# Kernel optimization log

Hardware: AMD Instinct MI355X
Metric: run time of the kernel (lower is better)

The kernel has to match this reference:

```python
import jax, jax.numpy as jnp
import numpy as np

N_SRC = 50000
N_DST = 50000
N_EDGES = 1600000
D_IN = 128
K = 8          # num_heads
D_OUT = 16     # out_dim per head (K*D_OUT = 128)
NEG_SLOPE = 0.2


def setup_inputs() -> dict:
    key = jax.random.key(0)
    ks = jax.random.split(key, 8)
    feat_src = jax.random.normal(ks[0], (N_SRC, D_IN), dtype=jnp.float32)
    feat_dst = jax.random.normal(ks[1], (N_DST, D_IN), dtype=jnp.float32)
    W_src = jax.random.normal(ks[2], (D_IN, K * D_OUT), dtype=jnp.float32) * (1.0 / np.sqrt(D_IN))
    b_src = jnp.zeros((K * D_OUT,), dtype=jnp.float32)
    W_dst = jax.random.normal(ks[3], (D_IN, K * D_OUT), dtype=jnp.float32) * (1.0 / np.sqrt(D_IN))
    b_dst = jnp.zeros((K * D_OUT,), dtype=jnp.float32)
    attn_src = jax.random.normal(ks[4], (K, 2 * D_OUT), dtype=jnp.float32) * 0.1
    src_idx = jax.random.randint(ks[5], (N_EDGES,), 0, N_SRC, dtype=jnp.int64)
    dst_idx = jax.random.randint(ks[6], (N_EDGES,), 0, N_DST, dtype=jnp.int64)
    return {"feat_src": feat_src, "feat_dst": feat_dst, "W_src": W_src, "b_src": b_src,
            "W_dst": W_dst, "b_dst": b_dst, "attn_src": attn_src,
            "src_idx": src_idx, "dst_idx": dst_idx}


def reference(feat_src, feat_dst, W_src, b_src, W_dst, b_dst, attn_src, src_idx, dst_idx):
    n_dst = feat_dst.shape[0]
    # feat_drop is identity (p=0). Linear projections, reshape to heads.
    hs = (feat_src @ W_src + b_src).reshape(-1, K, D_OUT)  # [N_src, K, D_out]
    hd = (feat_dst @ W_dst + b_dst).reshape(-1, K, D_OUT)  # [N_dst, K, D_out]
    # per-node attention logits
    el = jnp.sum(hs * attn_src[:, :D_OUT], axis=-1)  # [N_src, K]
    er = jnp.sum(hd * attn_src[:, D_OUT:], axis=-1)  # [N_dst, K]
    # per-edge score: u_add_v then LeakyReLU
    e = el[src_idx] + er[dst_idx]                    # [E, K]
    e = jnp.where(e >= 0, e, NEG_SLOPE * e)
    # edge softmax over incoming edges of each dst node (numerically stable)
    emax = jax.ops.segment_max(e, dst_idx, num_segments=n_dst)
    emax = jnp.where(jnp.isfinite(emax), emax, 0.0)  # handle dsts with no edges
    ee = jnp.exp(e - emax[dst_idx])                  # [E, K]
    esum = jax.ops.segment_sum(ee, dst_idx, num_segments=n_dst)
    a = ee / esum[dst_idx]                           # [E, K]
    # weighted message aggregation: u_mul_e then sum over incoming edges
    m = hs[src_idx] * a[:, :, None]                  # [E, K, D_out]
    out = jax.ops.segment_sum(m, dst_idx, num_segments=n_dst)  # [N_dst, K, D_out]
    return out.reshape(n_dst, K * D_OUT)
```

## Files before the change

### kernel.cpp

```cpp
#include <hip/hip_runtime.h>
#include <hip/hip_bf16.h>

#define NEG_SLOPE 0.2f
#define EPB   8192
#define CAP   4096
#define MAXC  1024

typedef __attribute__((ext_vector_type(8))) short bf16x8;
typedef __attribute__((ext_vector_type(4))) float f32x4;

__device__ __forceinline__ float b2f_lo(unsigned u) { return __uint_as_float(u << 16); }
__device__ __forceinline__ float b2f_hi(unsigned u) { return __uint_as_float(u & 0xffff0000u); }

__device__ __forceinline__ short f2b(float x) {
    unsigned u = __float_as_uint(x);
    unsigned r = (u + 0x7fffu + ((u >> 16) & 1u)) >> 16;
    return (short)r;
}

__global__ __launch_bounds__(256) void pack_kernel(
    const float* __restrict__ W_src, const float* __restrict__ W_dst,
    const float* __restrict__ b_src, const float* __restrict__ b_dst,
    const float* __restrict__ attn,
    uint4* __restrict__ wp_src, uint4* __restrict__ wp_dst,
    float* __restrict__ c_all,
    int* __restrict__ cursor, int nCoarse)
{
    const int e = blockIdx.x * 256 + threadIdx.x;
    if (e < 4608) {
        const int which = e / 2304;
        const int e2 = e % 2304;
        const float* W = which ? W_dst : W_src;
        uint4* wp = which ? wp_dst : wp_src;
        const int aoff = which ? 16 : 0;
        short out[8];
        if (e2 < 2048) {
            const int t = e2 >> 8, q = (e2 >> 6) & 3, l = e2 & 63;
            const int kbase = (l >> 4) * 8 + q * 32;
            const int n = t * 16 + (l & 15);
            #pragma unroll
            for (int j = 0; j < 8; ++j) out[j] = f2b(W[(size_t)(kbase + j) * 128 + n]);
            *(uint4*)&wp[(t * 4 + q) * 64 + l] = *(uint4*)out;
        } else {
            const int e3 = e2 - 2048;
            const int q = e3 >> 6, l = e3 & 63;
            const int kbase = (l >> 4) * 8 + q * 32;
            const int n = l & 15;
            #pragma unroll
            for (int j = 0; j < 8; ++j) {
                float v = 0.f;
                if (n < 8) {
                    for (int dd = 0; dd < 16; ++dd)
                        v += W[(size_t)(kbase + j) * 128 + n * 16 + dd] * attn[n * 32 + aoff + dd];
                }
                out[j] = f2b(v);
            }
            *(uint4*)&wp[(32 + q) * 64 + l] = *(uint4*)out;
        }
    } else if (e < 4624) {
        const int k = e - 4608;
        const int which = k >> 3, kk = k & 7;
        const float* bb = which ? b_dst : b_src;
        const int aoff = which ? 16 : 0;
        float v = 0.f;
        for (int dd = 0; dd < 16; ++dd) v += bb[kk * 16 + dd] * attn[kk * 32 + aoff + dd];
        c_all[k] = v;
    } else if (e < 4624 + nCoarse) {
        const int c = e - 4624;
        cursor[c] = c * CAP;
    }
}

__device__ __forceinline__ void scatter_body(
    const int* __restrict__ src_idx, const int* __restrict__ dst_idx,
    int* __restrict__ cursor, int* __restrict__ coarse,
    int nEdges, int nCoarse, int bx)
{
    __shared__ int lcnt[MAXC];
    __shared__ int lbase[MAXC];
    const int t = threadIdx.x;
    for (int i = t; i < nCoarse; i += 256) lcnt[i] = 0;
    __syncthreads();
    const int e0 = bx * EPB;
    const int e1 = min(e0 + EPB, nEdges);
    for (int e = e0 + t; e < e1; e += 256) atomicAdd(&lcnt[dst_idx[e] >> 6], 1);
    __syncthreads();
    for (int i = t; i < nCoarse; i += 256) {
        const int c = lcnt[i];
        lbase[i] = c ? atomicAdd(&cursor[i], c) : 0;
        lcnt[i] = 0;
    }
    __syncthreads();
    for (int e = e0 + t; e < e1; e += 256) {
        const int d = dst_idx[e];
        const int s = src_idx[e];
        const int bin = d >> 6;
        const int lr = atomicAdd(&lcnt[bin], 1);
        const int pos = lbase[bin] + lr;
        if (pos < (bin + 1) * CAP)
            coarse[pos] = (s << 6) | (d & 63);
    }
}

template<bool STORE_H>
__device__ __forceinline__ void proj_body(
    const float* __restrict__ feat, const uint4* __restrict__ wp,
    const float* __restrict__ b, const float* __restrict__ cvec,
    short* __restrict__ hs_out, float* __restrict__ el_out,
    int N, int bx)
{
    const int t = threadIdx.x;
    const int lane = t & 63;
    const int w = t >> 6;
    const int m  = lane & 15;
    const int q8 = lane >> 4;
    const int row0 = bx * 128 + w * 32;

    f32x4 acc0[9], acc1[9];
    #pragma unroll
    for (int tt = 0; tt < 8; ++tt) {
        const float bn = b[tt * 16 + m];
        acc0[tt] = (f32x4){bn, bn, bn, bn};
        acc1[tt] = (f32x4){bn, bn, bn, bn};
    }
    acc0[8] = (f32x4){0.f, 0.f, 0.f, 0.f};
    acc1[8] = (f32x4){0.f, 0.f, 0.f, 0.f};

    int rowA0 = row0 + m;      if (rowA0 >= N) rowA0 = N - 1;
    int rowA1 = row0 + 16 + m; if (rowA1 >= N) rowA1 = N - 1;
    const float* f0 = feat + (size_t)rowA0 * 128 + q8 * 8;
    const float* f1 = feat + (size_t)rowA1 * 128 + q8 * 8;
    const bf16x8* wpv = (const bf16x8*)wp;

    #pragma unroll
    for (int kc = 0; kc < 4; ++kc) {
        const float4 fa0 = *(const float4*)(f0 + kc * 32);
        const float4 fb0 = *(const float4*)(f0 + kc * 32 + 4);
        const float4 fa1 = *(const float4*)(f1 + kc * 32);
        const float4 fb1 = *(const float4*)(f1 + kc * 32 + 4);
        bf16x8 a0, a1;
        a0[0]=f2b(fa0.x); a0[1]=f2b(fa0.y); a0[2]=f2b(fa0.z); a0[3]=f2b(fa0.w);
        a0[4]=f2b(fb0.x); a0[5]=f2b(fb0.y); a0[6]=f2b(fb0.z); a0[7]=f2b(fb0.w);
        a1[0]=f2b(fa1.x); a1[1]=f2b(fa1.y); a1[2]=f2b(fa1.z); a1[3]=f2b(fa1.w);
        a1[4]=f2b(fb1.x); a1[5]=f2b(fb1.y); a1[6]=f2b(fb1.z); a1[7]=f2b(fb1.w);
        #pragma unroll
        for (int tt = 0; tt < 8; ++tt) {
            const bf16x8 bf = wpv[(tt * 4 + kc) * 64 + lane];
            acc0[tt] = __builtin_amdgcn_mfma_f32_16x16x32_bf16(a0, bf, acc0[tt], 0, 0, 0);
            acc1[tt] = __builtin_amdgcn_mfma_f32_16x16x32_bf16(a1, bf, acc1[tt], 0, 0, 0);
        }
        {
            const bf16x8 bv = wpv[(32 + kc) * 64 + lane];
            acc0[8] = __builtin_amdgcn_mfma_f32_16x16x32_bf16(a0, bv, acc0[8], 0, 0, 0);
            acc1[8] = __builtin_amdgcn_mfma_f32_16x16x32_bf16(a1, bv, acc1[8], 0, 0, 0);
        }
    }

    #pragma unroll
    for (int half = 0; half < 2; ++half) {
        const f32x4* acc = half ? acc1 : acc0;
        const int rbase = row0 + half * 16 + q8 * 4;
        #pragma unroll
        for (int reg = 0; reg < 4; ++reg) {
            const int row = rbase + reg;
            if (row < N) {
                if (STORE_H) {
                    #pragma unroll
                    for (int tt = 0; tt < 8; ++tt)
                        hs_out[(size_t)row * 128 + tt * 16 + m] = f2b(acc[tt][reg]);
                }
                if (m < 8) el_out[(size_t)row * 8 + m] = acc[8][reg] + cvec[m];
            }
        }
    }
}

__global__ __launch_bounds__(256, 2) void fused_kernel(
    const float* __restrict__ feat_src, const float* __restrict__ feat_dst,
    const uint4* __restrict__ wp_src, const uint4* __restrict__ wp_dst,
    const float* __restrict__ b_src, const float* __restrict__ b_dst,
    const float* __restrict__ c_all,
    short* __restrict__ hs, float* __restrict__ el, float* __restrict__ er,
    const int* __restrict__ src_idx, const int* __restrict__ dst_idx,
    int* __restrict__ cursor, int* __restrict__ coarse,
    int n_src, int n_dst, int nEdges, int nCoarse, int nSB, int pSrcBlocks)
{
    int bx = blockIdx.x;
    if (bx < nSB) { scatter_body(src_idx, dst_idx, cursor, coarse, nEdges, nCoarse, bx); return; }
    bx -= nSB;
    if (bx < pSrcBlocks) {
        proj_body<true>(feat_src, wp_src, b_src, c_all, hs, el, n_src, bx);
        return;
    }
    bx -= pSrcBlocks;
    proj_body<false>(feat_dst, wp_dst, b_dst, c_all + 8, nullptr, er, n_dst, bx);
}

__global__ __launch_bounds__(512) void sort_reduce_kernel(
    const int* __restrict__ coarse, const int* __restrict__ cursor,
    const float* __restrict__ el,
    const float* __restrict__ er,
    const unsigned short* __restrict__ hs,
    float* __restrict__ out,
    int n_dst, int nCoarse)
{
    __shared__ int fpk[CAP];
    __shared__ int h[64];
    __shared__ int lbeg[64];
    __shared__ int cu[64];
    __shared__ float erL[64 * 8];
    const int t = threadIdx.x, c = blockIdx.x;
    const int base_in = c * CAP;
    const int cnt = min(cursor[c] - base_in, CAP);

    if (t < 512) {
        const int d = c * 64 + (t >> 3);
        erL[t] = (d < n_dst) ? er[(size_t)d * 8 + (t & 7)] : 0.f;
    }
    if (t < 64) h[t] = 0;
    __syncthreads();
    for (int i = t; i < cnt; i += 512) atomicAdd(&h[coarse[base_in + i] & 63], 1);
    __syncthreads();
    if (t == 0) {
        int run = 0;
        #pragma unroll
        for (int j = 0; j < 64; ++j) { cu[j] = run; lbeg[j] = run; run += h[j]; }
    }
    __syncthreads();
    for (int i = t; i < cnt; i += 512) {
        const int v = coarse[base_in + i];
        const int p = atomicAdd(&cu[v & 63], 1);
        fpk[p] = v;
    }
    __syncthreads();

    const int w = t >> 6, lane = t & 63;
    const int sub = lane >> 5;
    const int l32 = lane & 31;
    const int k   = l32 >> 2;
    for (int j = 0; j < 8; ++j) {
        const int dl = w * 8 + j;
        const int d  = c * 64 + dl;
        if (d >= n_dst) break;
        const float erk = erL[dl * 8 + k];
        const int beg = lbeg[dl], end = lbeg[dl] + h[dl];
        float a0 = 0.f, a1 = 0.f, a2 = 0.f, a3 = 0.f, es = 0.f;
        int i = beg + sub;
        for (; i + 2 < end; i += 4) {
            const int sA = fpk[i] >> 6;
            const int sB = fpk[i + 2] >> 6;
            const float lA = el[(size_t)sA * 8 + k];
            const float lB = el[(size_t)sB * 8 + k];
            const uint2 uA = ((const uint2*)(hs + (size_t)sA * 128))[l32];
            const uint2 uB = ((const uint2*)(hs + (size_t)sB * 128))[l32];
            float xA = lA + erk; xA = (xA >= 0.f) ? xA : NEG_SLOPE * xA;
            float xB = lB + erk; xB = (xB >= 0.f) ? xB : NEG_SLOPE * xB;
            const float eA = __expf(xA);
            const float eB = __expf(xB);
            es += eA + eB;
            a0 = fmaf(eA, b2f_lo(uA.x), a0); a1 = fmaf(eA, b2f_hi(uA.x), a1);
            a2 = fmaf(eA, b2f_lo(uA.y), a2); a3 = fmaf(eA, b2f_hi(uA.y), a3);
            a0 = fmaf(eB, b2f_lo(uB.x), a0); a1 = fmaf(eB, b2f_hi(uB.x), a1);
            a2 = fmaf(eB, b2f_lo(uB.y), a2); a3 = fmaf(eB, b2f_hi(uB.y), a3);
        }
        for (; i < end; i += 2) {
            const int s = fpk[i] >> 6;
            const float l = el[(size_t)s * 8 + k];
            const uint2 u = ((const uint2*)(hs + (size_t)s * 128))[l32];
            float x = l + erk; x = (x >= 0.f) ? x : NEG_SLOPE * x;
            const float ee = __expf(x);
            es += ee;
            a0 = fmaf(ee, b2f_lo(u.x), a0); a1 = fmaf(ee, b2f_hi(u.x), a1);
            a2 = fmaf(ee, b2f_lo(u.y), a2); a3 = fmaf(ee, b2f_hi(u.y), a3);
        }
        es += __shfl_xor(es, 32);
        a0 += __shfl_xor(a0, 32);
        a1 += __shfl_xor(a1, 32);
        a2 += __shfl_xor(a2, 32);
        a3 += __shfl_xor(a3, 32);
        if (sub == 0) {
            const float inv = (es > 0.f) ? 1.f / es : 0.f;
            float4 o;
            o.x = a0 * inv; o.y = a1 * inv; o.z = a2 * inv; o.w = a3 * inv;
            *(float4*)(out + (size_t)d * 128 + l32 * 4) = o;
        }
    }
}

extern "C" void kernel_launch(void* const* d_in, const int* in_sizes, int n_in,
                              void* d_out, int out_size, void* d_ws, size_t ws_size,
                              hipStream_t stream) {
    const float* feat_src = (const float*)d_in[0];
    const float* feat_dst = (const float*)d_in[1];
    const float* W_src    = (const float*)d_in[2];
    const float* b_src    = (const float*)d_in[3];
    const float* W_dst    = (const float*)d_in[4];
    const float* b_dst    = (const float*)d_in[5];
    const float* attn     = (const float*)d_in[6];
    const int*   src_idx  = (const int*)d_in[7];
    const int*   dst_idx  = (const int*)d_in[8];
    float* out = (float*)d_out;

    const int n_src  = in_sizes[0] / 128;
    const int n_dst  = in_sizes[1] / 128;
    const int nEdges = in_sizes[7];

    const int nCoarse = (n_dst + 63) >> 6;
    const int nSB     = (nEdges + EPB - 1) / EPB;
    const int pSrc    = (n_src + 127) / 128;
    const int pDst    = (n_dst + 127) / 128;

    unsigned short* hs = (unsigned short*)d_ws;
    float* el = (float*)(hs + (size_t)n_src * 128);
    float* er = el + (size_t)n_src * 8;
    int* cursor = (int*)(er + (size_t)n_dst * 8);
    uintptr_t p = (uintptr_t)(cursor + nCoarse);
    p = (p + 15) & ~(uintptr_t)15;
    int* coarse = (int*)p;
    uintptr_t p2 = (uintptr_t)(coarse + (size_t)nCoarse * CAP);
    p2 = (p2 + 15) & ~(uintptr_t)15;
    uint4* wp_src = (uint4*)p2;
    uint4* wp_dst = wp_src + 36 * 64;
    float* c_all  = (float*)(wp_dst + 36 * 64);

    pack_kernel<<<22, 256, 0, stream>>>(W_src, W_dst, b_src, b_dst, attn,
                                        wp_src, wp_dst, c_all, cursor, nCoarse);

    fused_kernel<<<nSB + pSrc + pDst, 256, 0, stream>>>(
        feat_src, feat_dst, wp_src, wp_dst, b_src, b_dst, c_all,
        (short*)hs, el, er, src_idx, dst_idx, cursor, coarse,
        n_src, n_dst, nEdges, nCoarse, nSB, pSrc);

    sort_reduce_kernel<<<nCoarse, 512, 0, stream>>>(coarse, cursor, el, er,
                                                    hs, out, n_dst, nCoarse);
}
```

Before: 220.9 us.

## Replace coarse-bin sort with per-destination fixed-capacity edge arena

Edges are scattered straight into a per-destination slot arena (72 slots per destination) using one global atomic cursor per edge. This replaces the coarse 64-destination bins, which needed a local histogram, then a second in-block counting sort in the reduce kernel. The reduce kernel now reads source indices with 16-byte vector loads and unrolls four edges per half-wave, using smaller 256-thread blocks with 32 destinations each. In exchange it issues many more global atomics, and any edge beyond 72 for one destination is silently dropped.

```diff
diff --git a/kernel.cpp b/kernel.cpp
--- a/kernel.cpp
+++ b/kernel.cpp
@@ -3,8 +3,7 @@
 
 #define NEG_SLOPE 0.2f
 #define EPB   8192
-#define CAP   4096
-#define MAXC  1024
+#define CAP_D 72
 
 typedef __attribute__((ext_vector_type(8))) short bf16x8;
 typedef __attribute__((ext_vector_type(4))) float f32x4;
@@ -24,7 +23,7 @@
     const float* __restrict__ attn,
     uint4* __restrict__ wp_src, uint4* __restrict__ wp_dst,
     float* __restrict__ c_all,
-    int* __restrict__ cursor, int nCoarse)
+    int* __restrict__ cursor, int n_dst)
 {
     const int e = blockIdx.x * 256 + threadIdx.x;
     if (e < 4608) {
@@ -65,40 +64,26 @@
         float v = 0.f;
         for (int dd = 0; dd < 16; ++dd) v += bb[kk * 16 + dd] * attn[kk * 32 + aoff + dd];
         c_all[k] = v;
-    } else if (e < 4624 + nCoarse) {
-        const int c = e - 4624;
-        cursor[c] = c * CAP;
+    } else if (e < 4624 + n_dst) {
+        const int d = e - 4624;
+        cursor[d] = d * CAP_D;
     }
 }
 
 __device__ __forceinline__ void scatter_body(
     const int* __restrict__ src_idx, const int* __restrict__ dst_idx,
-    int* __restrict__ cursor, int* __restrict__ coarse,
-    int nEdges, int nCoarse, int bx)
-{
-    __shared__ int lcnt[MAXC];
-    __shared__ int lbase[MAXC];
+    int* __restrict__ cursor, int* __restrict__ arena,
+    int nEdges, int bx)
+{
     const int t = threadIdx.x;
-    for (int i = t; i < nCoarse; i += 256) lcnt[i] = 0;
-    __syncthreads();
     const int e0 = bx * EPB;
     const int e1 = min(e0 + EPB, nEdges);
-    for (int e = e0 + t; e < e1; e += 256) atomicAdd(&lcnt[dst_idx[e] >> 6], 1);
-    __syncthreads();
-    for (int i = t; i < nCoarse; i += 256) {
-        const int c = lcnt[i];
-        lbase[i] = c ? atomicAdd(&cursor[i], c) : 0;
-        lcnt[i] = 0;
-    }
-    __syncthreads();
     for (int e = e0 + t; e < e1; e += 256) {
         const int d = dst_idx[e];
         const int s = src_idx[e];
-        const int bin = d >> 6;
-        const int lr = atomicAdd(&lcnt[bin], 1);
-        const int pos = lbase[bin] + lr;
-        if (pos < (bin + 1) * CAP)
-            coarse[pos] = (s << 6) | (d & 63);
+        const int pos = atomicAdd(&cursor[d], 1);
+        if (pos < d * CAP_D + CAP_D)
+            arena[pos] = s;
     }
 }
 
@@ -182,11 +167,11 @@
     const float* __restrict__ c_all,
     short* __restrict__ hs, float* __restrict__ el, float* __restrict__ er,
     const int* __restrict__ src_idx, const int* __restrict__ dst_idx,
-    int* __restrict__ cursor, int* __restrict__ coarse,
-    int n_src, int n_dst, int nEdges, int nCoarse, int nSB, int pSrcBlocks)
+    int* __restrict__ cursor, int* __restrict__ arena,
+    int n_src, int n_dst, int nEdges, int nSB, int pSrcBlocks)
 {
     int bx = blockIdx.x;
-    if (bx < nSB) { scatter_body(src_idx, dst_idx, cursor, coarse, nEdges, nCoarse, bx); return; }
+    if (bx < nSB) { scatter_body(src_idx, dst_idx, cursor, arena, nEdges, bx); return; }
     bx -= nSB;
     if (bx < pSrcBlocks) {
         proj_body<true>(feat_src, wp_src, b_src, c_all, hs, el, n_src, bx);
@@ -196,41 +181,26 @@
     proj_body<false>(feat_dst, wp_dst, b_dst, c_all + 8, nullptr, er, n_dst, bx);
 }
 
-__global__ __launch_bounds__(512) void sort_reduce_kernel(
-    const int* __restrict__ coarse, const int* __restrict__ cursor,
+__global__ __launch_bounds__(256, 8) void gat_reduce_kernel(
+    const int* __restrict__ arena, const int* __restrict__ cursor,
     const float* __restrict__ el,
     const float* __restrict__ er,
     const unsigned short* __restrict__ hs,
     float* __restrict__ out,
-    int n_dst, int nCoarse)
-{
-    __shared__ int fpk[CAP];
-    __shared__ int h[64];
-    __shared__ int lbeg[64];
-    __shared__ int cu[64];
-    __shared__ float erL[64 * 8];
+    int n_dst)
+{
+    __shared__ float erL[32 * 8];
+    __shared__ int cntL[32];
     const int t = threadIdx.x, c = blockIdx.x;
-    const int base_in = c * CAP;
-    const int cnt = min(cursor[c] - base_in, CAP);
-
-    if (t < 512) {
-        const int d = c * 64 + (t >> 3);
+    const int d0 = c * 32;
+
+    {
+        const int d = d0 + (t >> 3);
         erL[t] = (d < n_dst) ? er[(size_t)d * 8 + (t & 7)] : 0.f;
-    }
-    if (t < 64) h[t] = 0;
-    __syncthreads();
-    for (int i = t; i < cnt; i += 512) atomicAdd(&h[coarse[base_in + i] & 63], 1);
-    __syncthreads();
-    if (t == 0) {
-        int run = 0;
-        #pragma unroll
-        for (int j = 0; j < 64; ++j) { cu[j] = run; lbeg[j] = run; run += h[j]; }
-    }
-    __syncthreads();
-    for (int i = t; i < cnt; i += 512) {
-        const int v = coarse[base_in + i];
-        const int p = atomicAdd(&cu[v & 63], 1);
-        fpk[p] = v;
+        if (t < 32) {
+            const int dd = d0 + t;
+            cntL[t] = (dd < n_dst) ? min(cursor[dd] - dd * CAP_D, CAP_D) : 0;
+        }
     }
     __syncthreads();
 
@@ -238,47 +208,64 @@
     const int sub = lane >> 5;
     const int l32 = lane & 31;
     const int k   = l32 >> 2;
+    const uint2* hs2 = (const uint2*)hs;
+
     for (int j = 0; j < 8; ++j) {
         const int dl = w * 8 + j;
-        const int d  = c * 64 + dl;
-        if (d >= n_dst) break;
+        const int d  = d0 + dl;
+        const int cnt = cntL[dl];
+        const int beg = d * CAP_D;
         const float erk = erL[dl * 8 + k];
-        const int beg = lbeg[dl], end = lbeg[dl] + h[dl];
         float a0 = 0.f, a1 = 0.f, a2 = 0.f, a3 = 0.f, es = 0.f;
-        int i = beg + sub;
-        for (; i + 2 < end; i += 4) {
-            const int sA = fpk[i] >> 6;
-            const int sB = fpk[i + 2] >> 6;
-            const float lA = el[(size_t)sA * 8 + k];
-            const float lB = el[(size_t)sB * 8 + k];
-            const uint2 uA = ((const uint2*)(hs + (size_t)sA * 128))[l32];
-            const uint2 uB = ((const uint2*)(hs + (size_t)sB * 128))[l32];
-            float xA = lA + erk; xA = (xA >= 0.f) ? xA : NEG_SLOPE * xA;
-            float xB = lB + erk; xB = (xB >= 0.f) ? xB : NEG_SLOPE * xB;
-            const float eA = __expf(xA);
-            const float eB = __expf(xB);
-            es += eA + eB;
-            a0 = fmaf(eA, b2f_lo(uA.x), a0); a1 = fmaf(eA, b2f_hi(uA.x), a1);
-            a2 = fmaf(eA, b2f_lo(uA.y), a2); a3 = fmaf(eA, b2f_hi(uA.y), a3);
-            a0 = fmaf(eB, b2f_lo(uB.x), a0); a1 = fmaf(eB, b2f_hi(uB.x), a1);
-            a2 = fmaf(eB, b2f_lo(uB.y), a2); a3 = fmaf(eB, b2f_hi(uB.y), a3);
-        }
-        for (; i < end; i += 2) {
-            const int s = fpk[i] >> 6;
-            const float l = el[(size_t)s * 8 + k];
-            const uint2 u = ((const uint2*)(hs + (size_t)s * 128))[l32];
-            float x = l + erk; x = (x >= 0.f) ? x : NEG_SLOPE * x;
+
+        int i = 4 * sub;
+        for (; i + 4 <= cnt; i += 8) {
+            const uint4 s4 = *(const uint4*)(arena + beg + i);
+            const int sa = (int)s4.x, sb = (int)s4.y, sc = (int)s4.z, sd = (int)s4.w;
+            const float lg0 = el[(size_t)sa * 8 + k];
+            const float lg1 = el[(size_t)sb * 8 + k];
+            const float lg2 = el[(size_t)sc * 8 + k];
+            const float lg3 = el[(size_t)sd * 8 + k];
+            const uint2 u0 = hs2[(size_t)sa * 32 + l32];
+            const uint2 u1 = hs2[(size_t)sb * 32 + l32];
+            const uint2 u2 = hs2[(size_t)sc * 32 + l32];
+            const uint2 u3 = hs2[(size_t)sd * 32 + l32];
+            float x0 = lg0 + erk; x0 = (x0 >= 0.f) ? x0 : NEG_SLOPE * x0;
+            float x1 = lg1 + erk; x1 = (x1 >= 0.f) ? x1 : NEG_SLOPE * x1;
+            float x2 = lg2 + erk; x2 = (x2 >= 0.f) ? x2 : NEG_SLOPE * x2;
+            float x3 = lg3 + erk; x3 = (x3 >= 0.f) ? x3 : NEG_SLOPE * x3;
+            const float e0 = __expf(x0);
+            const float e1 = __expf(x1);
+            const float e2 = __expf(x2);
+            const float e3 = __expf(x3);
+            es += (e0 + e1) + (e2 + e3);
+            a0 = fmaf(e0, b2f_lo(u0.x), a0); a1 = fmaf(e0, b2f_hi(u0.x), a1);
+            a2 = fmaf(e0, b2f_lo(u0.y), a2); a3 = fmaf(e0, b2f_hi(u0.y), a3);
+            a0 = fmaf(e1, b2f_lo(u1.x), a0); a1 = fmaf(e1, b2f_hi(u1.x), a1);
+            a2 = fmaf(e1, b2f_lo(u1.y), a2); a3 = fmaf(e1, b2f_hi(u1.y), a3);
+            a0 = fmaf(e2, b2f_lo(u2.x), a0); a1 = fmaf(e2, b2f_hi(u2.x), a1);
+            a2 = fmaf(e2, b2f_lo(u2.y), a2); a3 = fmaf(e2, b2f_hi(u2.y), a3);
+            a0 = fmaf(e3, b2f_lo(u3.x), a0); a1 = fmaf(e3, b2f_hi(u3.x), a1);
+            a2 = fmaf(e3, b2f_lo(u3.y), a2); a3 = fmaf(e3, b2f_hi(u3.y), a3);
+        }
+        const int iend = min(i + 4, cnt);
+        for (int i2 = i; i2 < iend; ++i2) {
+            const int s = arena[beg + i2];
+            const float lg = el[(size_t)s * 8 + k];
+            const uint2 u = hs2[(size_t)s * 32 + l32];
+            float x = lg + erk; x = (x >= 0.f) ? x : NEG_SLOPE * x;
             const float ee = __expf(x);
             es += ee;
             a0 = fmaf(ee, b2f_lo(u.x), a0); a1 = fmaf(ee, b2f_hi(u.x), a1);
             a2 = fmaf(ee, b2f_lo(u.y), a2); a3 = fmaf(ee, b2f_hi(u.y), a3);
         }
+
         es += __shfl_xor(es, 32);
         a0 += __shfl_xor(a0, 32);
         a1 += __shfl_xor(a1, 32);
         a2 += __shfl_xor(a2, 32);
         a3 += __shfl_xor(a3, 32);
-        if (sub == 0) {
+        if (sub == 0 && d < n_dst) {
             const float inv = (es > 0.f) ? 1.f / es : 0.f;
             float4 o;
             o.x = a0 * inv; o.y = a1 * inv; o.z = a2 * inv; o.w = a3 * inv;
@@ -305,32 +292,33 @@
     const int n_dst  = in_sizes[1] / 128;
     const int nEdges = in_sizes[7];
 
-    const int nCoarse = (n_dst + 63) >> 6;
-    const int nSB     = (nEdges + EPB - 1) / EPB;
-    const int pSrc    = (n_src + 127) / 128;
-    const int pDst    = (n_dst + 127) / 128;
+    const int nSB  = (nEdges + EPB - 1) / EPB;
+    const int pSrc = (n_src + 127) / 128;
+    const int pDst = (n_dst + 127) / 128;
+    const int nRB  = (n_dst + 31) / 32;
 
     unsigned short* hs = (unsigned short*)d_ws;
     float* el = (float*)(hs + (size_t)n_src * 128);
     float* er = el + (size_t)n_src * 8;
     int* cursor = (int*)(er + (size_t)n_dst * 8);
-    uintptr_t p = (uintptr_t)(cursor + nCoarse);
+    uintptr_t p = (uintptr_t)(cursor + n_dst);
     p = (p + 15) & ~(uintptr_t)15;
-    int* coarse = (int*)p;
-    uintptr_t p2 = (uintptr_t)(coarse + (size_t)nCoarse * CAP);
+    int* arena = (int*)p;
+    uintptr_t p2 = (uintptr_t)(arena + (size_t)n_dst * CAP_D);
     p2 = (p2 + 15) & ~(uintptr_t)15;
     uint4* wp_src = (uint4*)p2;
     uint4* wp_dst = wp_src + 36 * 64;
     float* c_all  = (float*)(wp_dst + 36 * 64);
 
-    pack_kernel<<<22, 256, 0, stream>>>(W_src, W_dst, b_src, b_dst, attn,
-                                        wp_src, wp_dst, c_all, cursor, nCoarse);
+    const int packBlocks = (4624 + n_dst + 255) / 256;
+    pack_kernel<<<packBlocks, 256, 0, stream>>>(W_src, W_dst, b_src, b_dst, attn,
+                                                wp_src, wp_dst, c_all, cursor, n_dst);
 
     fused_kernel<<<nSB + pSrc + pDst, 256, 0, stream>>>(
         feat_src, feat_dst, wp_src, wp_dst, b_src, b_dst, c_all,
-        (short*)hs, el, er, src_idx, dst_idx, cursor, coarse,
-        n_src, n_dst, nEdges, nCoarse, nSB, pSrc);
-
-    sort_reduce_kernel<<<nCoarse, 512, 0, stream>>>(coarse, cursor, el, er,
-                                                    hs, out, n_dst, nCoarse);
-}
+        (short*)hs, el, er, src_idx, dst_idx, cursor, arena,
+        n_src, n_dst, nEdges, nSB, pSrc);
+
+    gat_reduce_kernel<<<nRB, 256, 0, stream>>>(arena, cursor, el, er,
+                                               hs, out, n_dst);
+}
```

After: 277.7 us. 25.7% more time.

## Halve dst bin size to 32 and shrink sort-reduce blocks to 256 threads

Applied to the files above, without the earlier changes.

Coarse destination bins drop from 64 to 32 nodes, with capacity 2048 edges per bin, so the sort_reduce kernel runs twice as many 256-thread blocks that use less shared memory, aiming for more resident blocks per CU. Each thread now loads its bin entries into registers once instead of reading them twice from global memory, and the prefix sum over bin counts uses a warp shuffle scan instead of a serial loop. The pack kernel grid is sized from nCoarse so that all cursors get initialised. A smaller per-bin capacity makes overflow and dropped edges more likely on skewed degree distributions. The scatter's shared histogram also grows to 2048 bins.

```diff
diff --git a/kernel.cpp b/kernel.cpp
--- a/kernel.cpp
+++ b/kernel.cpp
@@ -3,8 +3,9 @@
 
 #define NEG_SLOPE 0.2f
 #define EPB   8192
-#define CAP   4096
-#define MAXC  1024
+#define BINSZ 32
+#define CAP   2048
+#define MAXC  2048
 
 typedef __attribute__((ext_vector_type(8))) short bf16x8;
 typedef __attribute__((ext_vector_type(4))) float f32x4;
@@ -83,7 +84,7 @@
     __syncthreads();
     const int e0 = bx * EPB;
     const int e1 = min(e0 + EPB, nEdges);
-    for (int e = e0 + t; e < e1; e += 256) atomicAdd(&lcnt[dst_idx[e] >> 6], 1);
+    for (int e = e0 + t; e < e1; e += 256) atomicAdd(&lcnt[dst_idx[e] >> 5], 1);
     __syncthreads();
     for (int i = t; i < nCoarse; i += 256) {
         const int c = lcnt[i];
@@ -94,11 +95,11 @@
     for (int e = e0 + t; e < e1; e += 256) {
         const int d = dst_idx[e];
         const int s = src_idx[e];
-        const int bin = d >> 6;
+        const int bin = d >> 5;
         const int lr = atomicAdd(&lcnt[bin], 1);
         const int pos = lbase[bin] + lr;
         if (pos < (bin + 1) * CAP)
-            coarse[pos] = (s << 6) | (d & 63);
+            coarse[pos] = (s << 5) | (d & 31);
     }
 }
 
@@ -196,7 +197,7 @@
     proj_body<false>(feat_dst, wp_dst, b_dst, c_all + 8, nullptr, er, n_dst, bx);
 }
 
-__global__ __launch_bounds__(512) void sort_reduce_kernel(
+__global__ __launch_bounds__(256, 8) void sort_reduce_kernel(
     const int* __restrict__ coarse, const int* __restrict__ cursor,
     const float* __restrict__ el,
     const float* __restrict__ er,
@@ -205,54 +206,71 @@
     int n_dst, int nCoarse)
 {
     __shared__ int fpk[CAP];
-    __shared__ int h[64];
-    __shared__ int lbeg[64];
-    __shared__ int cu[64];
-    __shared__ float erL[64 * 8];
+    __shared__ int h[BINSZ];
+    __shared__ int lbeg[BINSZ];
+    __shared__ int cu[BINSZ];
+    __shared__ float erL[BINSZ * 8];
     const int t = threadIdx.x, c = blockIdx.x;
     const int base_in = c * CAP;
     const int cnt = min(cursor[c] - base_in, CAP);
 
-    if (t < 512) {
-        const int d = c * 64 + (t >> 3);
+    {
+        const int d = c * BINSZ + (t >> 3);
         erL[t] = (d < n_dst) ? er[(size_t)d * 8 + (t & 7)] : 0.f;
     }
-    if (t < 64) h[t] = 0;
-    __syncthreads();
-    for (int i = t; i < cnt; i += 512) atomicAdd(&h[coarse[base_in + i] & 63], 1);
-    __syncthreads();
-    if (t == 0) {
-        int run = 0;
+    if (t < BINSZ) h[t] = 0;
+    __syncthreads();
+
+    int ev[8];
+    #pragma unroll
+    for (int r = 0; r < 8; ++r) {
+        const int idx = t + (r << 8);
+        ev[r] = (idx < cnt) ? coarse[base_in + idx] : -1;
+    }
+    #pragma unroll
+    for (int r = 0; r < 8; ++r)
+        if (ev[r] >= 0) atomicAdd(&h[ev[r] & 31], 1);
+    __syncthreads();
+    if (t < BINSZ) {
+        const int v = h[t];
+        int sc = v;
         #pragma unroll
-        for (int j = 0; j < 64; ++j) { cu[j] = run; lbeg[j] = run; run += h[j]; }
-    }
-    __syncthreads();
-    for (int i = t; i < cnt; i += 512) {
-        const int v = coarse[base_in + i];
-        const int p = atomicAdd(&cu[v & 63], 1);
-        fpk[p] = v;
-    }
+        for (int off = 1; off < BINSZ; off <<= 1) {
+            const int nb = __shfl_up(sc, off);
+            if (t >= off) sc += nb;
+        }
+        lbeg[t] = sc - v;
+        cu[t]   = sc - v;
+    }
+    __syncthreads();
+    #pragma unroll
+    for (int r = 0; r < 8; ++r)
+        if (ev[r] >= 0) {
+            const int p = atomicAdd(&cu[ev[r] & 31], 1);
+            fpk[p] = ev[r];
+        }
     __syncthreads();
 
     const int w = t >> 6, lane = t & 63;
     const int sub = lane >> 5;
     const int l32 = lane & 31;
     const int k   = l32 >> 2;
+    const uint2* hs2 = (const uint2*)hs;
     for (int j = 0; j < 8; ++j) {
         const int dl = w * 8 + j;
-        const int d  = c * 64 + dl;
+        const int d  = c * BINSZ + dl;
         if (d >= n_dst) break;
         const float erk = erL[dl * 8 + k];
         const int beg = lbeg[dl], end = lbeg[dl] + h[dl];
         float a0 = 0.f, a1 = 0.f, a2 = 0.f, a3 = 0.f, es = 0.f;
         int i = beg + sub;
         for (; i + 2 < end; i += 4) {
-            const int sA = fpk[i] >> 6;
-            const int sB = fpk[i + 2] >> 6;
+            const int sA = fpk[i] >> 5;
+            const int sB = fpk[i + 2] >> 5;
             const float lA = el[(size_t)sA * 8 + k];
             const float lB = el[(size_t)sB * 8 + k];
-            const uint2 uA = ((const uint2*)(hs + (size_t)sA * 128))[l32];
-            const uint2 uB = ((const uint2*)(hs + (size_t)sB * 128))[l32];
+            const uint2 uA = hs2[(size_t)sA * 32 + l32];
+            const uint2 uB = hs2[(size_t)sB * 32 + l32];
             float xA = lA + erk; xA = (xA >= 0.f) ? xA : NEG_SLOPE * xA;
             float xB = lB + erk; xB = (xB >= 0.f) ? xB : NEG_SLOPE * xB;
             const float eA = __expf(xA);
@@ -264,9 +282,9 @@
             a2 = fmaf(eB, b2f_lo(uB.y), a2); a3 = fmaf(eB, b2f_hi(uB.y), a3);
         }
         for (; i < end; i += 2) {
-            const int s = fpk[i] >> 6;
+            const int s = fpk[i] >> 5;
             const float l = el[(size_t)s * 8 + k];
-            const uint2 u = ((const uint2*)(hs + (size_t)s * 128))[l32];
+            const uint2 u = hs2[(size_t)s * 32 + l32];
             float x = l + erk; x = (x >= 0.f) ? x : NEG_SLOPE * x;
             const float ee = __expf(x);
             es += ee;
@@ -305,7 +323,7 @@
     const int n_dst  = in_sizes[1] / 128;
     const int nEdges = in_sizes[7];
 
-    const int nCoarse = (n_dst + 63) >> 6;
+    const int nCoarse = (n_dst + BINSZ - 1) / BINSZ;
     const int nSB     = (nEdges + EPB - 1) / EPB;
     const int pSrc    = (n_src + 127) / 128;
     const int pDst    = (n_dst + 127) / 128;
@@ -323,14 +341,15 @@
     uint4* wp_dst = wp_src + 36 * 64;
     float* c_all  = (float*)(wp_dst + 36 * 64);
 
-    pack_kernel<<<22, 256, 0, stream>>>(W_src, W_dst, b_src, b_dst, attn,
-                                        wp_src, wp_dst, c_all, cursor, nCoarse);
+    const int packBlocks = (4624 + nCoarse + 255) / 256;
+    pack_kernel<<<packBlocks, 256, 0, stream>>>(W_src, W_dst, b_src, b_dst, attn,
+                                                wp_src, wp_dst, c_all, cursor, nCoarse);
 
     fused_kernel<<<nSB + pSrc + pDst, 256, 0, stream>>>(
         feat_src, feat_dst, wp_src, wp_dst, b_src, b_dst, c_all,
         (short*)hs, el, er, src_idx, dst_idx, cursor, coarse,
         n_src, n_dst, nEdges, nCoarse, nSB, pSrc);
 
-    sort_reduce_kernel<<<nCoarse, 512, 0, stream>>>(coarse, cursor, el, er,
+    sort_reduce_kernel<<<nCoarse, 256, 0, stream>>>(coarse, cursor, el, er,
                                                     hs, out, n_dst, nCoarse);
 }
```

Result: faster. 214.4 us (-3.0%).
